# Performance work log

Hardware: AMD Instinct MI355X
Metric: run time of the kernel (lower is better)

The kernel has to match this reference:

```python
import jax, jax.numpy as jnp
import numpy as np

# Label indices assumed by the original module's transition init
SAME, NEW1, NEW2, BACK, OFF = 0, 1, 2, 3, 4


def _init_transitions(n=5):
    T = np.zeros((n, n), np.float32)
    T[SAME, SAME] += 0.8
    for y in (NEW1, NEW2):
        T[SAME, y] -= 0.2
        T[y, SAME] += 0.3
    T[NEW1, NEW2] -= 0.5
    T[NEW2, NEW1] -= 0.5
    for y in (NEW1, NEW2):
        T[BACK, y] += 0.2
    for c in range(n):
        T[OFF, c] -= 0.3
        T[c, OFF] -= 0.3
    return jnp.asarray(T)


def setup_inputs() -> dict:
    key = jax.random.key(0)
    kZ, kW, kt, ks, ke = jax.random.split(key, 5)
    B, L, D, C = 32, 2048, 512, 5
    Z = jax.random.normal(kZ, (B, L, D), jnp.float32)
    tags = jax.random.randint(kt, (B, L), 0, C)
    mask_u = jnp.ones((B, L), dtype=bool)  # first timestep must be on (torchcrf requirement)
    W = jax.random.normal(kW, (C, D), jnp.float32) * 0.02
    b = jnp.zeros((C,), jnp.float32)
    class_bias = jnp.array([0.0, 0.15, 0.15, 0.0, 0.15], jnp.float32)
    start_trans = jax.random.uniform(ks, (C,), jnp.float32, -0.1, 0.1)
    end_trans = jax.random.uniform(ke, (C,), jnp.float32, -0.1, 0.1)
    transitions = _init_transitions(C)
    return dict(Z=Z, tags=tags, mask_u=mask_u, W=W, b=b, class_bias=class_bias,
                start_trans=start_trans, end_trans=end_trans, transitions=transitions)


def _crf_nll_mean(em, tags, mask, start_t, end_t, trans):
    # em: [B,L,C], tags/mask: [B,L]. Returns -mean_b log p(tags_b | em_b) (torchcrf reduction='mean').
    B, L, C = em.shape
    maskf = mask.astype(em.dtype)
    # --- numerator: score of the gold path ---
    em_tag = jnp.take_along_axis(em, tags[..., None], axis=2)[..., 0]            # [B,L]
    trans_sc = trans[tags[:, :-1], tags[:, 1:]]                                  # [B,L-1]
    lengths = mask.sum(axis=1)                                                   # [B]
    last_tags = jnp.take_along_axis(tags, (lengths - 1)[:, None], axis=1)[:, 0]  # [B]
    numerator = (start_t[tags[:, 0]] + em_tag[:, 0]
                 + jnp.sum((trans_sc + em_tag[:, 1:]) * maskf[:, 1:], axis=1)
                 + end_t[last_tags])                                             # [B]
    # --- denominator: log partition via forward algorithm (single fused scan) ---
    alpha0 = start_t[None, :] + em[:, 0]                                         # [B,C]
    em_rest = jnp.swapaxes(em[:, 1:], 0, 1)                                      # [L-1,B,C]
    m_rest = jnp.swapaxes(mask[:, 1:], 0, 1)                                     # [L-1,B]

    def step(alpha, x):
        e, m = x
        nxt = jax.nn.logsumexp(alpha[:, :, None] + trans[None, :, :] + e[:, None, :], axis=1)
        return jnp.where(m[:, None], nxt, alpha), None

    alpha, _ = jax.lax.scan(step, alpha0, (em_rest, m_rest))
    log_z = jax.nn.logsumexp(alpha + end_t[None, :], axis=1)                     # [B]
    return -jnp.mean(numerator - log_z)


def reference(Z, tags, mask_u, W, b, class_bias, start_trans, end_trans, transitions):
    # emissions(): dropout is identity in eval mode
    em = Z @ W.T + b + class_bias                                                # [B,L,5]
    return _crf_nll_mean(em, tags, mask_u, start_trans, end_trans, transitions)
```

## Files before the change

### kernel.cpp

```cpp
#include <hip/hip_runtime.h>
#include <hip/hip_bf16.h>

#define BB 32
#define LL 2048
#define DD 512
#define CC 5
#define CH 128
#define NCH (LL / CH)
#define NSUB 16
#define SUBLEN (CH / NSUB)

static __device__ __forceinline__ float lse5(float v0, float v1, float v2,
                                             float v3, float v4) {
    const float LOG2E = 1.4426950408889634f;
    const float LN2   = 0.6931471805599453f;
    float m = fmaxf(fmaxf(fmaxf(v0, v1), fmaxf(v2, v3)), v4);
    float s = exp2f((v0 - m) * LOG2E) + exp2f((v1 - m) * LOG2E)
            + exp2f((v2 - m) * LOG2E) + exp2f((v3 - m) * LOG2E)
            + exp2f((v4 - m) * LOG2E);
    return m + log2f(s) * LN2;
}


__global__ __launch_bounds__(512) void fused_kernel(
    const float* __restrict__ Z, const int* __restrict__ tags,
    const float* __restrict__ W, const float* __restrict__ bias,
    const float* __restrict__ cbias, const float* __restrict__ start_t,
    const float* __restrict__ end_t, const float* __restrict__ trans,
    float* __restrict__ Pw, float* __restrict__ alpha0w,
    float* __restrict__ numw) {
    __shared__ float em_s[CH * CC];
    __shared__ float Q_s[NSUB][25];

    const int g   = blockIdx.x;
    const int b   = blockIdx.y;
    const int tid = threadIdx.x;
    const int wv  = tid >> 6;
    const int lane = tid & 63;
    const int t0  = g * CH;

    {
        const int colb = lane * 8;
        float4 w0[CC], w1[CC];
        float bc[CC];
#pragma unroll
        for (int c = 0; c < CC; ++c) {
            w0[c] = *(const float4*)(W + c * DD + colb);
            w1[c] = *(const float4*)(W + c * DD + colb + 4);
            bc[c] = bias[c] + cbias[c];
        }
        const float* zbase = Z + ((size_t)(b * LL + t0 + wv * 16)) * DD + colb;
#pragma unroll 2
        for (int i = 0; i < 16; ++i) {
            const float* zr = zbase + (size_t)i * DD;
            float4 z0 = *(const float4*)(zr);
            float4 z1 = *(const float4*)(zr + 4);
            float acc[CC];
#pragma unroll
            for (int c = 0; c < CC; ++c) {
                acc[c] = z0.x * w0[c].x + z0.y * w0[c].y
                       + z0.z * w0[c].z + z0.w * w0[c].w
                       + z1.x * w1[c].x + z1.y * w1[c].y
                       + z1.z * w1[c].z + z1.w * w1[c].w;
            }
#pragma unroll
            for (int off = 32; off >= 1; off >>= 1)
#pragma unroll
                for (int c = 0; c < CC; ++c)
                    acc[c] += __shfl_xor(acc[c], off, 64);
            if (lane == 0) {
                int r = wv * 16 + i;
#pragma unroll
                for (int c = 0; c < CC; ++c)
                    em_s[r * CC + c] = acc[c] + bc[c];
            }
        }
    }
    __syncthreads();

    const int* tg = tags + b * LL;

    if (tid < CH) {
        int t = t0 + tid;
        int tag = tg[t];
        float num = em_s[tid * CC + tag];
        if (t >= 1) num += trans[tg[t - 1] * CC + tag];
        else        num += start_t[tag];
        if (t == LL - 1) num += end_t[tag];
#pragma unroll
        for (int off = 32; off >= 1; off >>= 1)
            num += __shfl_xor(num, off, 64);
        if (lane == 0) numw[(b * NCH + g) * 2 + wv] = num;
    }
    if (g == 0 && tid < CC)
        alpha0w[b * CC + tid] = start_t[tid] + em_s[tid];

    const int grp = tid >> 5;
    const int l32 = tid & 31;
    if (l32 < 25) {
        const int p = l32 / 5, c = l32 % 5;
        float tcol[CC];
#pragma unroll
        for (int q = 0; q < CC; ++q) tcol[q] = trans[q * CC + c];

        int ts = grp * SUBLEN + ((g == 0 && grp == 0) ? 1 : 0);
        int te = grp * SUBLEN + SUBLEN;
        float a = trans[p * CC + c] + em_s[ts * CC + c];
        for (int t = ts + 1; t < te; ++t) {
            float v0 = __shfl(a, p * 5 + 0, 32) + tcol[0];
            float v1 = __shfl(a, p * 5 + 1, 32) + tcol[1];
            float v2 = __shfl(a, p * 5 + 2, 32) + tcol[2];
            float v3 = __shfl(a, p * 5 + 3, 32) + tcol[3];
            float v4 = __shfl(a, p * 5 + 4, 32) + tcol[4];
            a = lse5(v0, v1, v2, v3, v4) + em_s[t * CC + c];
        }
        Q_s[grp][l32] = a;
    }
    __syncthreads();

    if (tid < 32 && l32 < 25) {
        const int p = l32 / 5, c = l32 % 5;
        float a = Q_s[0][l32];
        for (int j = 1; j < NSUB; ++j) {
            float v0 = __shfl(a, p * 5 + 0, 32) + Q_s[j][0 * 5 + c];
            float v1 = __shfl(a, p * 5 + 1, 32) + Q_s[j][1 * 5 + c];
            float v2 = __shfl(a, p * 5 + 2, 32) + Q_s[j][2 * 5 + c];
            float v3 = __shfl(a, p * 5 + 3, 32) + Q_s[j][3 * 5 + c];
            float v4 = __shfl(a, p * 5 + 4, 32) + Q_s[j][4 * 5 + c];
            a = lse5(v0, v1, v2, v3, v4);
        }
        Pw[(b * NCH + g) * 25 + l32] = a;
    }
}

__global__ __launch_bounds__(1024) void fold_kernel(
    const float* __restrict__ Pw, const float* __restrict__ alpha0w,
    const float* __restrict__ numw, const float* __restrict__ end_t,
    float* __restrict__ out) {
    __shared__ float P_s[BB * NCH * 25];
    __shared__ float res_s[BB];

    int tid = threadIdx.x;
    for (int i = tid; i < BB * NCH * 25; i += 1024) P_s[i] = Pw[i];
    __syncthreads();

    int grp = tid >> 5;
    int l32 = tid & 31;
    int c = (l32 < 5) ? l32 : 0;

    float alpha = alpha0w[grp * CC + c];
    const float* Pb = P_s + grp * NCH * 25;
    for (int j = 0; j < NCH; ++j) {
        const float* Pj = Pb + j * 25;
        float v0 = __shfl(alpha, 0, 32) + Pj[0 * 5 + c];
        float v1 = __shfl(alpha, 1, 32) + Pj[1 * 5 + c];
        float v2 = __shfl(alpha, 2, 32) + Pj[2 * 5 + c];
        float v3 = __shfl(alpha, 3, 32) + Pj[3 * 5 + c];
        float v4 = __shfl(alpha, 4, 32) + Pj[4 * 5 + c];
        alpha = lse5(v0, v1, v2, v3, v4);
    }
    alpha += end_t[c];

    float num = numw[grp * 32 + l32];
#pragma unroll
    for (int off = 16; off >= 1; off >>= 1)
        num += __shfl_xor(num, off, 32);

    float v0 = __shfl(alpha, 0, 32);
    float v1 = __shfl(alpha, 1, 32);
    float v2 = __shfl(alpha, 2, 32);
    float v3 = __shfl(alpha, 3, 32);
    float v4 = __shfl(alpha, 4, 32);
    if (l32 == 0)
        res_s[grp] = lse5(v0, v1, v2, v3, v4) - num;
    __syncthreads();

    if (tid == 0) {
        float s = 0.f;
        for (int bb = 0; bb < BB; ++bb) s += res_s[bb];
        out[0] = s / (float)BB;
    }
}

extern "C" void kernel_launch(void* const* d_in, const int* in_sizes, int n_in,
                              void* d_out, int out_size, void* d_ws, size_t ws_size,
                              hipStream_t stream) {
    const float* Z       = (const float*)d_in[0];
    const int*   tags    = (const int*)d_in[1];
    const float* W       = (const float*)d_in[3];
    const float* bias    = (const float*)d_in[4];
    const float* cbias   = (const float*)d_in[5];
    const float* start_t = (const float*)d_in[6];
    const float* end_t   = (const float*)d_in[7];
    const float* trans   = (const float*)d_in[8];

    float* wsf     = (float*)d_ws;
    float* Pw      = wsf;
    float* alpha0w = wsf + BB * NCH * 25;
    float* numw    = alpha0w + BB * CC;
    float* out     = (float*)d_out;

    fused_kernel<<<dim3(NCH, BB), 512, 0, stream>>>(
        Z, tags, W, bias, cbias, start_t, end_t, trans, Pw, alpha0w, numw);
    fold_kernel<<<1, 1024, 0, stream>>>(Pw, alpha0w, numw, end_t, out);
}
```

Before: 52.37 us.

## Compute emission projection with bf16 MFMA instead of FP32 dot-product shuffles

Replaces the per-row FP32 dot product and 6-level cross-lane shuffle reduction with a 16x16x32 bf16 MFMA. Each wave converts Z rows to bf16 in registers and multiplies them against W staged as bf16 in shared memory. The emission buffer layout becomes class-major to match the MFMA output. This removes the shuffle-reduction overhead but lowers precision to bf16 inputs and adds a W staging pass and an extra barrier per block; the kernel stays bound by reading Z from memory.

```diff
diff --git a/kernel.cpp b/kernel.cpp
--- a/kernel.cpp
+++ b/kernel.cpp
@@ -9,6 +9,14 @@
 #define NCH (LL / CH)
 #define NSUB 16
 #define SUBLEN (CH / NSUB)
+
+typedef __attribute__((ext_vector_type(8))) short short8;
+typedef __attribute__((ext_vector_type(4))) float f32x4;
+
+static __device__ __forceinline__ unsigned short f2bf(float x) {
+    __bf16 h = (__bf16)x;
+    return __builtin_bit_cast(unsigned short, h);
+}
 
 static __device__ __forceinline__ float lse5(float v0, float v1, float v2,
                                              float v3, float v4) {
@@ -29,7 +37,8 @@
     const float* __restrict__ end_t, const float* __restrict__ trans,
     float* __restrict__ Pw, float* __restrict__ alpha0w,
     float* __restrict__ numw) {
-    __shared__ float em_s[CH * CC];
+    __shared__ __align__(16) unsigned short W_s[CC][520];
+    __shared__ __align__(16) float em_s[CC][132];
     __shared__ float Q_s[NSUB][25];
 
     const int g   = blockIdx.x;
@@ -39,41 +48,35 @@
     const int lane = tid & 63;
     const int t0  = g * CH;
 
+    for (int i = tid; i < CC * DD; i += 512)
+        W_s[i >> 9][i & 511] = f2bf(W[i]);
+    __syncthreads();
+
     {
-        const int colb = lane * 8;
-        float4 w0[CC], w1[CC];
-        float bc[CC];
-#pragma unroll
-        for (int c = 0; c < CC; ++c) {
-            w0[c] = *(const float4*)(W + c * DD + colb);
-            w1[c] = *(const float4*)(W + c * DD + colb + 4);
-            bc[c] = bias[c] + cbias[c];
-        }
-        const float* zbase = Z + ((size_t)(b * LL + t0 + wv * 16)) * DD + colb;
-#pragma unroll 2
-        for (int i = 0; i < 16; ++i) {
-            const float* zr = zbase + (size_t)i * DD;
-            float4 z0 = *(const float4*)(zr);
-            float4 z1 = *(const float4*)(zr + 4);
-            float acc[CC];
-#pragma unroll
-            for (int c = 0; c < CC; ++c) {
-                acc[c] = z0.x * w0[c].x + z0.y * w0[c].y
-                       + z0.z * w0[c].z + z0.w * w0[c].w
-                       + z1.x * w1[c].x + z1.y * w1[c].y
-                       + z1.z * w1[c].z + z1.w * w1[c].w;
-            }
-#pragma unroll
-            for (int off = 32; off >= 1; off >>= 1)
-#pragma unroll
-                for (int c = 0; c < CC; ++c)
-                    acc[c] += __shfl_xor(acc[c], off, 64);
-            if (lane == 0) {
-                int r = wv * 16 + i;
-#pragma unroll
-                for (int c = 0; c < CC; ++c)
-                    em_s[r * CC + c] = acc[c] + bc[c];
-            }
+        const int r16 = lane & 15;
+        const int g16 = lane >> 4;
+        const float* zrow = Z + ((size_t)b * LL + t0 + wv * 16 + r16) * DD
+                          + g16 * 8;
+        const int nsel = (r16 < CC) ? r16 : (CC - 1);
+        const unsigned short* wrow = &W_s[nsel][g16 * 8];
+
+        f32x4 acc = {0.f, 0.f, 0.f, 0.f};
+#pragma unroll
+        for (int s = 0; s < 16; ++s) {
+            float4 z0 = *(const float4*)(zrow + 32 * s);
+            float4 z1 = *(const float4*)(zrow + 32 * s + 4);
+            short8 a;
+            a[0] = (short)f2bf(z0.x); a[1] = (short)f2bf(z0.y);
+            a[2] = (short)f2bf(z0.z); a[3] = (short)f2bf(z0.w);
+            a[4] = (short)f2bf(z1.x); a[5] = (short)f2bf(z1.y);
+            a[6] = (short)f2bf(z1.z); a[7] = (short)f2bf(z1.w);
+            short8 bf = *(const short8*)(wrow + 32 * s);
+            acc = __builtin_amdgcn_mfma_f32_16x16x32_bf16(a, bf, acc, 0, 0, 0);
+        }
+        if (r16 < CC) {
+            float bc = bias[r16] + cbias[r16];
+            acc[0] += bc; acc[1] += bc; acc[2] += bc; acc[3] += bc;
+            *(f32x4*)&em_s[r16][wv * 16 + g16 * 4] = acc;
         }
     }
     __syncthreads();
@@ -83,7 +86,7 @@
     if (tid < CH) {
         int t = t0 + tid;
         int tag = tg[t];
-        float num = em_s[tid * CC + tag];
+        float num = em_s[tag][tid];
         if (t >= 1) num += trans[tg[t - 1] * CC + tag];
         else        num += start_t[tag];
         if (t == LL - 1) num += end_t[tag];
@@ -93,7 +96,7 @@
         if (lane == 0) numw[(b * NCH + g) * 2 + wv] = num;
     }
     if (g == 0 && tid < CC)
-        alpha0w[b * CC + tid] = start_t[tid] + em_s[tid];
+        alpha0w[b * CC + tid] = start_t[tid] + em_s[tid][0];
 
     const int grp = tid >> 5;
     const int l32 = tid & 31;
@@ -105,14 +108,14 @@
 
         int ts = grp * SUBLEN + ((g == 0 && grp == 0) ? 1 : 0);
         int te = grp * SUBLEN + SUBLEN;
-        float a = trans[p * CC + c] + em_s[ts * CC + c];
+        float a = trans[p * CC + c] + em_s[c][ts];
         for (int t = ts + 1; t < te; ++t) {
             float v0 = __shfl(a, p * 5 + 0, 32) + tcol[0];
             float v1 = __shfl(a, p * 5 + 1, 32) + tcol[1];
             float v2 = __shfl(a, p * 5 + 2, 32) + tcol[2];
             float v3 = __shfl(a, p * 5 + 3, 32) + tcol[3];
             float v4 = __shfl(a, p * 5 + 4, 32) + tcol[4];
-            a = lse5(v0, v1, v2, v3, v4) + em_s[t * CC + c];
+            a = lse5(v0, v1, v2, v3, v4) + em_s[c][t];
         }
         Q_s[grp][l32] = a;
     }
```

New measurement: 46.12 us. -11.9%, faster.
